# Kernel optimization log

Hardware: AMD Instinct MI355X
Metric: run time of the kernel (lower is better)

Reference implementation:

```python
import jax, jax.numpy as jnp
import numpy as np


def adder2d(x, w, stride=1, padding=0):
    """AdderNet conv: out = -sum_{ci,kh,kw} |x_patch - w|, supports groups.
    x: [B,Cin,H,W], w: [Cout, Cin//G, K, K]. Loops only over K*K kernel taps."""
    B, Cin, H, W = x.shape
    Cout, Cin_g, K, _ = w.shape
    G = Cin // Cin_g
    Co_g = Cout // G
    xp = jnp.pad(x, ((0, 0), (0, 0), (padding, padding), (padding, padding)))
    Ho = (H + 2 * padding - K) // stride + 1
    Wo = (W + 2 * padding - K) // stride + 1
    wg = w.reshape(G, Co_g, Cin_g, K, K)
    out = jnp.zeros((B, Cout, Ho, Wo), x.dtype)
    for kh in range(K):
        for kw in range(K):
            xs = jax.lax.slice(
                xp, (0, 0, kh, kw),
                (B, Cin, kh + stride * (Ho - 1) + 1, kw + stride * (Wo - 1) + 1),
                (1, 1, stride, stride))  # [B,Cin,Ho,Wo]
            xs = xs.reshape(B, G, 1, Cin_g, Ho, Wo)
            wt = wg[:, :, :, kh, kw][None, :, :, :, None, None]  # [1,G,Co_g,Cin_g,1,1]
            out = out - jnp.abs(xs - wt).sum(3).reshape(B, Cout, Ho, Wo)
    return out


def bn(x, g, b, m, v, eps=1e-5):
    inv = g / jnp.sqrt(v + eps)
    return x * inv[None, :, None, None] + (b - m * inv)[None, :, None, None]


def setup_inputs() -> dict:
    key = jax.random.key(0)
    ks = jax.random.split(key, 18)
    d = {}
    d["x"] = jax.random.normal(ks[0], (8, 256, 28, 28), jnp.float32)
    d["w1"] = jax.random.normal(ks[1], (64, 256, 1, 1), jnp.float32) * 0.05
    d["w_peg"] = jax.random.normal(ks[2], (64, 1, 3, 3), jnp.float32) * 0.05
    d["w2"] = jax.random.normal(ks[3], (64, 64, 3, 3), jnp.float32) * 0.05
    d["w3"] = jax.random.normal(ks[4], (256, 64, 1, 1), jnp.float32) * 0.05
    for i, (c, tag) in enumerate([(64, "1"), (64, "2"), (256, "3")]):
        d["g" + tag] = jax.random.uniform(ks[5 + 4 * i], (c,), jnp.float32, 0.5, 1.5)
        d["b" + tag] = jax.random.normal(ks[6 + 4 * i], (c,), jnp.float32) * 0.1
        d["m" + tag] = jax.random.normal(ks[7 + 4 * i], (c,), jnp.float32) * 0.1
        d["v" + tag] = jax.random.uniform(ks[8 + 4 * i], (c,), jnp.float32, 0.5, 1.5)
    return d


def reference(x, w1, w_peg, w2, w3, g1, b1, m1, v1, g2, b2, m2, v2, g3, b3, m3, v3):
    residual = x  # downsample is Identity (stride=1, inplanes==outplanes)
    h = adder2d(x, w1)                       # 1x1 adder conv 256->64
    h = adder2d(h, w_peg, stride=1, padding=1)  # PEG: depthwise 3x3 adder conv
    h = jax.nn.relu(bn(h, g1, b1, m1, v1))
    h = adder2d(h, w2, padding=1)            # 3x3 adder conv 64->64
    h = jax.nn.relu(bn(h, g2, b2, m2, v2))
    h = adder2d(h, w3)                       # 1x1 adder conv 64->256
    h = bn(h, g3, b3, m3, v3)
    return jax.nn.relu(h + residual)
```

## Files before the change

### kernel.cpp

```cpp
#include <hip/hip_runtime.h>
#include <math.h>

#define HW 28
#define PR 30
#define PC 32
#define PPAD (PR * PC)

#define OFF_H1P 0
#define OFF_H2P 491520
#define OFF_H3  983040
#define OFF_W2T 1384448
#define OFF_W3T 1421312
#define OFF_W1T 1437696

__device__ __forceinline__ void tap3(const float4 a, const float2 b,
                                     const float w0, const float w1, const float w2,
                                     float4& acc) {
    acc.x += fabsf(a.x - w0) + fabsf(a.y - w1) + fabsf(a.z - w2);
    acc.y += fabsf(a.y - w0) + fabsf(a.z - w1) + fabsf(a.w - w2);
    acc.z += fabsf(a.z - w0) + fabsf(a.w - w1) + fabsf(b.x - w2);
    acc.w += fabsf(a.w - w0) + fabsf(b.x - w1) + fabsf(b.y - w2);
}

__global__ __launch_bounds__(256) void k0_setup(const float* __restrict__ w1,
                                                const float* __restrict__ w2,
                                                const float* __restrict__ w3,
                                                float* __restrict__ w1t,
                                                float* __restrict__ w2t,
                                                float* __restrict__ w3t,
                                                float* __restrict__ h1p,
                                                float* __restrict__ h2p) {
    int t = blockIdx.x * 256 + threadIdx.x;
    if (t < 16384) {
        int ci = t >> 6, co = t & 63;
        w1t[t] = w1[co * 256 + ci];
    } else if (t < 53248) {
        int r2 = t - 16384;
        int r = r2 >> 6, co = r2 & 63;
        w2t[r2] = w2[(size_t)co * 576 + r];
    } else if (t < 69632) {
        int r3 = t - 53248;
        int ci = r3 >> 8, co = r3 & 255;
        w3t[r3] = w3[co * 64 + ci];
    } else {
        int h = t - 69632;
        float* buf = (h < 90112) ? h1p : h2p;
        int rem = (h < 90112) ? h : h - 90112;
        int plane = rem / 176, r = rem % 176;
        int row, col;
        if (r < 64) { row = (r >> 5) * 29; col = r & 31; }
        else { int j = r - 64; row = 1 + (j >> 2); int k = j & 3; col = k ? 28 + k : 0; }
        buf[(size_t)plane * PPAD + row * PC + col] = 0.f;
    }
}

__global__ __launch_bounds__(448) void k1_adder1x1(const float* __restrict__ x,
                                                   const float* __restrict__ w1t,
                                                   float* __restrict__ h1p) {
    __shared__ __align__(16) float smem[7168];
    float*  ws  = smem;
    float4* pl4 = (float4*)smem;
    const int tid    = threadIdx.x;
    const int cog    = tid & 3;
    const int pxg    = (tid >> 2) % 7;
    const int cic    = tid / 28;
    const int n      = blockIdx.x / 28;
    const int y      = blockIdx.x % 28;
    const int px0    = y * 28 + pxg * 4;
    const int cobase = blockIdx.y * 16;

    for (int idx = tid; idx < 4096; idx += 448) {
        int ci = idx >> 4, co = idx & 15;
        ws[ci * 20 + co] = w1t[ci * 64 + cobase + co];
    }
    __syncthreads();

    float4 acc0 = {0,0,0,0}, acc1 = acc0, acc2 = acc0, acc3 = acc0;
    const float* xp = x + ((size_t)n * 256 + cic * 16) * 784 + px0;
    const float* wp = ws + (cic * 16) * 20 + cog * 4;
    #pragma unroll 8
    for (int i = 0; i < 16; ++i) {
        float4 u = *(const float4*)(xp + (size_t)i * 784);
        float4 w = *(const float4*)(wp + i * 20);
        acc0.x += fabsf(u.x - w.x); acc0.y += fabsf(u.y - w.x); acc0.z += fabsf(u.z - w.x); acc0.w += fabsf(u.w - w.x);
        acc1.x += fabsf(u.x - w.y); acc1.y += fabsf(u.y - w.y); acc1.z += fabsf(u.z - w.y); acc1.w += fabsf(u.w - w.y);
        acc2.x += fabsf(u.x - w.z); acc2.y += fabsf(u.y - w.z); acc2.z += fabsf(u.z - w.z); acc2.w += fabsf(u.w - w.z);
        acc3.x += fabsf(u.x - w.w); acc3.y += fabsf(u.y - w.w); acc3.z += fabsf(u.z - w.w); acc3.w += fabsf(u.w - w.w);
    }
    __syncthreads();
    const int pbase = pxg * 16 + cog * 4;
    pl4[cic * 112 + pbase + 0] = acc0;
    pl4[cic * 112 + pbase + 1] = acc1;
    pl4[cic * 112 + pbase + 2] = acc2;
    pl4[cic * 112 + pbase + 3] = acc3;
    __syncthreads();

    if (tid < 112) {
        const int rpxg = tid >> 4;
        const int rcog = (tid >> 2) & 3;
        const int j    = tid & 3;
        const int rb   = rpxg * 16 + rcog * 4 + j;
        float4 s = pl4[rb];
        #pragma unroll
        for (int c = 1; c < 16; ++c) {
            float4 t = pl4[c * 112 + rb];
            s.x += t.x; s.y += t.y; s.z += t.z; s.w += t.w;
        }
        const int co = cobase + rcog * 4 + j;
        float* op = h1p + ((size_t)(n * 64 + co) * PR + y + 1) * PC + rpxg * 4 + 1;
        op[0] = -s.x; op[1] = -s.y; op[2] = -s.z; op[3] = -s.w;
    }
}

__global__ __launch_bounds__(256) void k2_peg_bn_relu(const float* __restrict__ h1p,
                                                      const float* __restrict__ wp,
                                                      const float* __restrict__ g1,
                                                      const float* __restrict__ b1,
                                                      const float* __restrict__ m1,
                                                      const float* __restrict__ v1,
                                                      float* __restrict__ h2p) {
    const int t   = blockIdx.x * 256 + threadIdx.x;
    const int pxq = t % 196;
    const int c   = (t / 196) & 63;
    const int n   = t / (196 * 64);
    const int p0  = pxq * 4;
    const int y   = p0 / 28, xx = p0 % 28;

    const float* base = h1p + ((size_t)(n * 64 + c) * PR + y) * PC + xx;
    const float* wc   = wp + c * 9;
    float4 acc = {0,0,0,0};
    #pragma unroll
    for (int kh = 0; kh < 3; ++kh) {
        float4 a = *(const float4*)(base + kh * PC);
        float2 b = *(const float2*)(base + kh * PC + 4);
        tap3(a, b, wc[kh * 3 + 0], wc[kh * 3 + 1], wc[kh * 3 + 2], acc);
    }
    float inv = g1[c] * rsqrtf(v1[c] + 1e-5f);
    float bb  = b1[c] - m1[c] * inv;
    float* op = h2p + ((size_t)(n * 64 + c) * PR + y + 1) * PC + xx + 1;
    op[0] = fmaxf(-acc.x * inv + bb, 0.f);
    op[1] = fmaxf(-acc.y * inv + bb, 0.f);
    op[2] = fmaxf(-acc.z * inv + bb, 0.f);
    op[3] = fmaxf(-acc.w * inv + bb, 0.f);
}

__global__ __launch_bounds__(448) void k3_adder3x3_bn_relu(const float* __restrict__ h2p,
                                                           const float* __restrict__ w2t,
                                                           const float* __restrict__ g2,
                                                           const float* __restrict__ b2,
                                                           const float* __restrict__ m2,
                                                           const float* __restrict__ v2,
                                                           float* __restrict__ h3) {
    __shared__ __align__(16) float smem[9216];
    float*  ws  = smem;
    float4* pl4 = (float4*)smem;
    const int tid    = threadIdx.x;
    const int cog    = tid & 3;
    const int pxg    = (tid >> 2) % 7;
    const int cic    = tid / 28;
    const int Y      = blockIdx.x;
    const int cobase = blockIdx.y * 16;
    const int n      = blockIdx.z;
    const int xx0    = pxg * 4;

    #pragma unroll
    for (int k = 0; k < 21; ++k) {
        int idx = tid + k * 448;
        if (idx < 9216) ws[idx] = w2t[(size_t)(idx >> 4) * 64 + cobase + (idx & 15)];
    }
    __syncthreads();

    float4 acc0 = {0,0,0,0}, acc1 = acc0, acc2 = acc0, acc3 = acc0;
    #pragma unroll 2
    for (int i = 0; i < 4; ++i) {
        const int ci = cic * 4 + i;
        const float* rp = h2p + (((size_t)(n * 64 + ci)) * PR + Y) * PC + xx0;
        const float* wr = ws + ci * 144 + cog * 4;
        #pragma unroll
        for (int kh = 0; kh < 3; ++kh) {
            float4 a = *(const float4*)(rp + kh * PC);
            float2 b = *(const float2*)(rp + kh * PC + 4);
            const float* wk = wr + kh * 48;
            float4 W0 = *(const float4*)(wk);
            float4 W1 = *(const float4*)(wk + 16);
            float4 W2 = *(const float4*)(wk + 32);
            tap3(a, b, W0.x, W1.x, W2.x, acc0);
            tap3(a, b, W0.y, W1.y, W2.y, acc1);
            tap3(a, b, W0.z, W1.z, W2.z, acc2);
            tap3(a, b, W0.w, W1.w, W2.w, acc3);
        }
    }
    __syncthreads();
    const int pbase = pxg * 16 + cog * 4;
    pl4[cic * 112 + pbase + 0] = acc0;
    pl4[cic * 112 + pbase + 1] = acc1;
    pl4[cic * 112 + pbase + 2] = acc2;
    pl4[cic * 112 + pbase + 3] = acc3;
    __syncthreads();

    if (tid < 112) {
        const int rpxg = tid >> 4;
        const int rcog = (tid >> 2) & 3;
        const int j    = tid & 3;
        const int rb   = rpxg * 16 + rcog * 4 + j;
        float4 s = pl4[rb];
        #pragma unroll
        for (int c = 1; c < 16; ++c) {
            float4 t = pl4[c * 112 + rb];
            s.x += t.x; s.y += t.y; s.z += t.z; s.w += t.w;
        }
        const int co = cobase + rcog * 4 + j;
        float inv = g2[co] * rsqrtf(v2[co] + 1e-5f);
        float bb  = b2[co] - m2[co] * inv;
        float4 o;
        o.x = fmaxf(-s.x * inv + bb, 0.f);
        o.y = fmaxf(-s.y * inv + bb, 0.f);
        o.z = fmaxf(-s.z * inv + bb, 0.f);
        o.w = fmaxf(-s.w * inv + bb, 0.f);
        *(float4*)(h3 + (size_t)(n * 64 + co) * 784 + Y * 28 + rpxg * 4) = o;
    }
}

__global__ __launch_bounds__(448) void k6_adder1x1_bn_res_relu(const float* __restrict__ h3,
                                                               const float* __restrict__ w3t,
                                                               const float* __restrict__ x,
                                                               const float* __restrict__ g3,
                                                               const float* __restrict__ b3,
                                                               const float* __restrict__ m3,
                                                               const float* __restrict__ v3,
                                                               float* __restrict__ out) {
    __shared__ __align__(16) float smem[7168];
    float*  ws  = smem;
    float4* pl4 = (float4*)smem;
    const int tid    = threadIdx.x;
    const int cog    = tid & 7;
    const int pxg    = (tid >> 3) % 14;
    const int cic    = tid / 112;
    const int n      = blockIdx.x / 14;
    const int p0     = (blockIdx.x % 14) * 56 + pxg * 4;
    const int cobase = blockIdx.y * 32;

    for (int idx = tid; idx < 2048; idx += 448) {
        int ci = idx >> 5, co = idx & 31;
        ws[ci * 36 + co] = w3t[ci * 256 + cobase + co];
    }
    __syncthreads();

    float4 acc0 = {0,0,0,0}, acc1 = acc0, acc2 = acc0, acc3 = acc0;
    const float* hp = h3 + ((size_t)n * 64 + cic * 16) * 784 + p0;
    const float* wp = ws + (cic * 16) * 36 + cog * 4;
    #pragma unroll 8
    for (int i = 0; i < 16; ++i) {
        float4 u = *(const float4*)(hp + (size_t)i * 784);
        float4 w = *(const float4*)(wp + i * 36);
        acc0.x += fabsf(u.x - w.x); acc0.y += fabsf(u.y - w.x); acc0.z += fabsf(u.z - w.x); acc0.w += fabsf(u.w - w.x);
        acc1.x += fabsf(u.x - w.y); acc1.y += fabsf(u.y - w.y); acc1.z += fabsf(u.z - w.y); acc1.w += fabsf(u.w - w.y);
        acc2.x += fabsf(u.x - w.z); acc2.y += fabsf(u.y - w.z); acc2.z += fabsf(u.z - w.z); acc2.w += fabsf(u.w - w.z);
        acc3.x += fabsf(u.x - w.w); acc3.y += fabsf(u.y - w.w); acc3.z += fabsf(u.z - w.w); acc3.w += fabsf(u.w - w.w);
    }
    __syncthreads();
    const int pbase = pxg * 32 + cog * 4;
    pl4[cic * 448 + pbase + 0] = acc0;
    pl4[cic * 448 + pbase + 1] = acc1;
    pl4[cic * 448 + pbase + 2] = acc2;
    pl4[cic * 448 + pbase + 3] = acc3;
    __syncthreads();

    {
        const int j = cic;
        float4 s = pl4[pbase + j];
        #pragma unroll
        for (int c = 1; c < 4; ++c) {
            float4 t = pl4[c * 448 + pbase + j];
            s.x += t.x; s.y += t.y; s.z += t.z; s.w += t.w;
        }
        const int co = cobase + cog * 4 + j;
        float inv = g3[co] * rsqrtf(v3[co] + 1e-5f);
        float bb  = b3[co] - m3[co] * inv;
        size_t obase = ((size_t)n * 256 + co) * 784 + p0;
        float4 r = *(const float4*)(x + obase);
        float4 o;
        o.x = fmaxf(-s.x * inv + bb + r.x, 0.f);
        o.y = fmaxf(-s.y * inv + bb + r.y, 0.f);
        o.z = fmaxf(-s.z * inv + bb + r.z, 0.f);
        o.w = fmaxf(-s.w * inv + bb + r.w, 0.f);
        *(float4*)(out + obase) = o;
    }
}

extern "C" void kernel_launch(void* const* d_in, const int* in_sizes, int n_in,
                              void* d_out, int out_size, void* d_ws, size_t ws_size,
                              hipStream_t stream) {
    const float* x  = (const float*)d_in[0];
    const float* w1 = (const float*)d_in[1];
    const float* wp = (const float*)d_in[2];
    const float* w2 = (const float*)d_in[3];
    const float* w3 = (const float*)d_in[4];
    const float* g1 = (const float*)d_in[5];
    const float* b1 = (const float*)d_in[6];
    const float* m1 = (const float*)d_in[7];
    const float* v1 = (const float*)d_in[8];
    const float* g2 = (const float*)d_in[9];
    const float* b2 = (const float*)d_in[10];
    const float* m2 = (const float*)d_in[11];
    const float* v2 = (const float*)d_in[12];
    const float* g3 = (const float*)d_in[13];
    const float* b3 = (const float*)d_in[14];
    const float* m3 = (const float*)d_in[15];
    const float* v3 = (const float*)d_in[16];
    float* out = (float*)d_out;

    float* wsf = (float*)d_ws;
    float* h1p = wsf + OFF_H1P;
    float* h2p = wsf + OFF_H2P;
    float* h3  = wsf + OFF_H3;
    float* w2t = wsf + OFF_W2T;
    float* w3t = wsf + OFF_W3T;
    float* w1t = wsf + OFF_W1T;

    k0_setup<<<dim3(976), 256, 0, stream>>>(w1, w2, w3, w1t, w2t, w3t, h1p, h2p);
    k1_adder1x1<<<dim3(224, 4), 448, 0, stream>>>(x, w1t, h1p);
    k2_peg_bn_relu<<<dim3(392), 256, 0, stream>>>(h1p, wp, g1, b1, m1, v1, h2p);
    k3_adder3x3_bn_relu<<<dim3(28, 4, 8), 448, 0, stream>>>(h2p, w2t, g2, b2, m2, v2, h3);
    k6_adder1x1_bn_res_relu<<<dim3(112, 8), 448, 0, stream>>>(h3, w3t, x, g3, b3, m3, v3, out);
}
```

Baseline: 69.81 us.

## Drop setup kernel; fold weight transposes and halo zeroing into consumers, retile 3x3

```diff
diff --git a/kernel.cpp b/kernel.cpp
--- a/kernel.cpp
+++ b/kernel.cpp
@@ -9,9 +9,6 @@
 #define OFF_H1P 0
 #define OFF_H2P 491520
 #define OFF_H3  983040
-#define OFF_W2T 1384448
-#define OFF_W3T 1421312
-#define OFF_W1T 1437696
 
 __device__ __forceinline__ void tap3(const float4 a, const float2 b,
                                      const float w0, const float w1, const float w2,
@@ -22,40 +19,8 @@
     acc.w += fabsf(a.w - w0) + fabsf(b.x - w1) + fabsf(b.y - w2);
 }
 
-__global__ __launch_bounds__(256) void k0_setup(const float* __restrict__ w1,
-                                                const float* __restrict__ w2,
-                                                const float* __restrict__ w3,
-                                                float* __restrict__ w1t,
-                                                float* __restrict__ w2t,
-                                                float* __restrict__ w3t,
-                                                float* __restrict__ h1p,
-                                                float* __restrict__ h2p) {
-    int t = blockIdx.x * 256 + threadIdx.x;
-    if (t < 16384) {
-        int ci = t >> 6, co = t & 63;
-        w1t[t] = w1[co * 256 + ci];
-    } else if (t < 53248) {
-        int r2 = t - 16384;
-        int r = r2 >> 6, co = r2 & 63;
-        w2t[r2] = w2[(size_t)co * 576 + r];
-    } else if (t < 69632) {
-        int r3 = t - 53248;
-        int ci = r3 >> 8, co = r3 & 255;
-        w3t[r3] = w3[co * 64 + ci];
-    } else {
-        int h = t - 69632;
-        float* buf = (h < 90112) ? h1p : h2p;
-        int rem = (h < 90112) ? h : h - 90112;
-        int plane = rem / 176, r = rem % 176;
-        int row, col;
-        if (r < 64) { row = (r >> 5) * 29; col = r & 31; }
-        else { int j = r - 64; row = 1 + (j >> 2); int k = j & 3; col = k ? 28 + k : 0; }
-        buf[(size_t)plane * PPAD + row * PC + col] = 0.f;
-    }
-}
-
 __global__ __launch_bounds__(448) void k1_adder1x1(const float* __restrict__ x,
-                                                   const float* __restrict__ w1t,
+                                                   const float* __restrict__ w1,
                                                    float* __restrict__ h1p) {
     __shared__ __align__(16) float smem[7168];
     float*  ws  = smem;
@@ -70,8 +35,8 @@
     const int cobase = blockIdx.y * 16;
 
     for (int idx = tid; idx < 4096; idx += 448) {
-        int ci = idx >> 4, co = idx & 15;
-        ws[ci * 20 + co] = w1t[ci * 64 + cobase + co];
+        int co = idx >> 8, ci = idx & 255;
+        ws[ci * 20 + co] = w1[(size_t)(cobase + co) * 256 + ci];
     }
     __syncthreads();
 
@@ -109,6 +74,15 @@
         const int co = cobase + rcog * 4 + j;
         float* op = h1p + ((size_t)(n * 64 + co) * PR + y + 1) * PC + rpxg * 4 + 1;
         op[0] = -s.x; op[1] = -s.y; op[2] = -s.z; op[3] = -s.w;
+        if (rpxg == 0) op[-1] = 0.f;
+        if (rpxg == 6) { op[4] = 0.f; op[5] = 0.f; op[6] = 0.f; }
+    }
+    if (y == 0 || y == 27) {
+        const int prow = (y == 0) ? 0 : 29;
+        for (int idx = tid; idx < 512; idx += 448) {
+            int coi = idx >> 5, col = idx & 31;
+            h1p[((size_t)(n * 64 + cobase + coi) * PR + prow) * PC + col] = 0.f;
+        }
     }
 }
 
@@ -119,71 +93,81 @@
                                                       const float* __restrict__ m1,
                                                       const float* __restrict__ v1,
                                                       float* __restrict__ h2p) {
-    const int t   = blockIdx.x * 256 + threadIdx.x;
-    const int pxq = t % 196;
-    const int c   = (t / 196) & 63;
-    const int n   = t / (196 * 64);
-    const int p0  = pxq * 4;
-    const int y   = p0 / 28, xx = p0 % 28;
-
-    const float* base = h1p + ((size_t)(n * 64 + c) * PR + y) * PC + xx;
-    const float* wc   = wp + c * 9;
-    float4 acc = {0,0,0,0};
-    #pragma unroll
-    for (int kh = 0; kh < 3; ++kh) {
-        float4 a = *(const float4*)(base + kh * PC);
-        float2 b = *(const float2*)(base + kh * PC + 4);
-        tap3(a, b, wc[kh * 3 + 0], wc[kh * 3 + 1], wc[kh * 3 + 2], acc);
-    }
-    float inv = g1[c] * rsqrtf(v1[c] + 1e-5f);
-    float bb  = b1[c] - m1[c] * inv;
-    float* op = h2p + ((size_t)(n * 64 + c) * PR + y + 1) * PC + xx + 1;
-    op[0] = fmaxf(-acc.x * inv + bb, 0.f);
-    op[1] = fmaxf(-acc.y * inv + bb, 0.f);
-    op[2] = fmaxf(-acc.z * inv + bb, 0.f);
-    op[3] = fmaxf(-acc.w * inv + bb, 0.f);
+    const int t = blockIdx.x * 256 + threadIdx.x;
+    if (t < 100352) {
+        const int pxq = t % 196;
+        const int c   = (t / 196) & 63;
+        const int n   = t / (196 * 64);
+        const int p0  = pxq * 4;
+        const int y   = p0 / 28, xx = p0 % 28;
+        const float* base = h1p + ((size_t)(n * 64 + c) * PR + y) * PC + xx;
+        const float* wc   = wp + c * 9;
+        float4 acc = {0,0,0,0};
+        #pragma unroll
+        for (int kh = 0; kh < 3; ++kh) {
+            float4 a = *(const float4*)(base + kh * PC);
+            float2 b = *(const float2*)(base + kh * PC + 4);
+            tap3(a, b, wc[kh * 3 + 0], wc[kh * 3 + 1], wc[kh * 3 + 2], acc);
+        }
+        float inv = g1[c] * rsqrtf(v1[c] + 1e-5f);
+        float bb  = b1[c] - m1[c] * inv;
+        float* op = h2p + ((size_t)(n * 64 + c) * PR + y + 1) * PC + xx + 1;
+        op[0] = fmaxf(-acc.x * inv + bb, 0.f);
+        op[1] = fmaxf(-acc.y * inv + bb, 0.f);
+        op[2] = fmaxf(-acc.z * inv + bb, 0.f);
+        op[3] = fmaxf(-acc.w * inv + bb, 0.f);
+    } else {
+        int i = t - 100352;
+        int plane = i / 176, r = i % 176;
+        int row, col;
+        if (r < 64) { row = (r >> 5) * 29; col = r & 31; }
+        else { int j = r - 64; row = 1 + (j >> 2); int k = j & 3; col = k ? 28 + k : 0; }
+        h2p[(size_t)plane * PPAD + row * PC + col] = 0.f;
+    }
 }
 
 __global__ __launch_bounds__(448) void k3_adder3x3_bn_relu(const float* __restrict__ h2p,
-                                                           const float* __restrict__ w2t,
+                                                           const float* __restrict__ w2,
                                                            const float* __restrict__ g2,
                                                            const float* __restrict__ b2,
                                                            const float* __restrict__ m2,
                                                            const float* __restrict__ v2,
                                                            float* __restrict__ h3) {
-    __shared__ __align__(16) float smem[9216];
+    __shared__ __align__(16) float smem[11520];
     float*  ws  = smem;
     float4* pl4 = (float4*)smem;
     const int tid    = threadIdx.x;
     const int cog    = tid & 3;
-    const int pxg    = (tid >> 2) % 7;
-    const int cic    = tid / 28;
-    const int Y      = blockIdx.x;
+    const int pxg    = (tid >> 2) % 14;
+    const int cic    = tid / 56;
+    const int y0     = blockIdx.x * 2;
     const int cobase = blockIdx.y * 16;
     const int n      = blockIdx.z;
-    const int xx0    = pxg * 4;
-
-    #pragma unroll
-    for (int k = 0; k < 21; ++k) {
-        int idx = tid + k * 448;
-        if (idx < 9216) ws[idx] = w2t[(size_t)(idx >> 4) * 64 + cobase + (idx & 15)];
+    const int yl     = pxg / 7;
+    const int xx0    = (pxg % 7) * 4;
+    const int Y      = y0 + yl;
+
+    for (int idx = tid; idx < 9216; idx += 448) {
+        int co = idx / 576;
+        int r  = idx - co * 576;
+        ws[r * 20 + co] = w2[(size_t)(cobase + co) * 576 + r];
     }
     __syncthreads();
 
     float4 acc0 = {0,0,0,0}, acc1 = acc0, acc2 = acc0, acc3 = acc0;
     #pragma unroll 2
-    for (int i = 0; i < 4; ++i) {
-        const int ci = cic * 4 + i;
+    for (int i = 0; i < 8; ++i) {
+        const int ci = cic * 8 + i;
         const float* rp = h2p + (((size_t)(n * 64 + ci)) * PR + Y) * PC + xx0;
-        const float* wr = ws + ci * 144 + cog * 4;
+        const float* wr = ws + ci * 180 + cog * 4;
         #pragma unroll
         for (int kh = 0; kh < 3; ++kh) {
             float4 a = *(const float4*)(rp + kh * PC);
             float2 b = *(const float2*)(rp + kh * PC + 4);
-            const float* wk = wr + kh * 48;
+            const float* wk = wr + kh * 60;
             float4 W0 = *(const float4*)(wk);
-            float4 W1 = *(const float4*)(wk + 16);
-            float4 W2 = *(const float4*)(wk + 32);
+            float4 W1 = *(const float4*)(wk + 20);
+            float4 W2 = *(const float4*)(wk + 40);
             tap3(a, b, W0.x, W1.x, W2.x, acc0);
             tap3(a, b, W0.y, W1.y, W2.y, acc1);
             tap3(a, b, W0.z, W1.z, W2.z, acc2);
@@ -192,24 +176,21 @@
     }
     __syncthreads();
     const int pbase = pxg * 16 + cog * 4;
-    pl4[cic * 112 + pbase + 0] = acc0;
-    pl4[cic * 112 + pbase + 1] = acc1;
-    pl4[cic * 112 + pbase + 2] = acc2;
-    pl4[cic * 112 + pbase + 3] = acc3;
-    __syncthreads();
-
-    if (tid < 112) {
-        const int rpxg = tid >> 4;
-        const int rcog = (tid >> 2) & 3;
-        const int j    = tid & 3;
-        const int rb   = rpxg * 16 + rcog * 4 + j;
-        float4 s = pl4[rb];
-        #pragma unroll
-        for (int c = 1; c < 16; ++c) {
-            float4 t = pl4[c * 112 + rb];
+    pl4[cic * 224 + pbase + 0] = acc0;
+    pl4[cic * 224 + pbase + 1] = acc1;
+    pl4[cic * 224 + pbase + 2] = acc2;
+    pl4[cic * 224 + pbase + 3] = acc3;
+    __syncthreads();
+
+    if (tid < 224) {
+        const int j = cic;
+        float4 s = pl4[pbase + j];
+        #pragma unroll
+        for (int c = 1; c < 8; ++c) {
+            float4 t = pl4[c * 224 + pbase + j];
             s.x += t.x; s.y += t.y; s.z += t.z; s.w += t.w;
         }
-        const int co = cobase + rcog * 4 + j;
+        const int co = cobase + cog * 4 + j;
         float inv = g2[co] * rsqrtf(v2[co] + 1e-5f);
         float bb  = b2[co] - m2[co] * inv;
         float4 o;
@@ -217,12 +198,12 @@
         o.y = fmaxf(-s.y * inv + bb, 0.f);
         o.z = fmaxf(-s.z * inv + bb, 0.f);
         o.w = fmaxf(-s.w * inv + bb, 0.f);
-        *(float4*)(h3 + (size_t)(n * 64 + co) * 784 + Y * 28 + rpxg * 4) = o;
+        *(float4*)(h3 + (size_t)(n * 64 + co) * 784 + Y * 28 + xx0) = o;
     }
 }
 
 __global__ __launch_bounds__(448) void k6_adder1x1_bn_res_relu(const float* __restrict__ h3,
-                                                               const float* __restrict__ w3t,
+                                                               const float* __restrict__ w3,
                                                                const float* __restrict__ x,
                                                                const float* __restrict__ g3,
                                                                const float* __restrict__ b3,
@@ -241,8 +222,8 @@
     const int cobase = blockIdx.y * 32;
 
     for (int idx = tid; idx < 2048; idx += 448) {
-        int ci = idx >> 5, co = idx & 31;
-        ws[ci * 36 + co] = w3t[ci * 256 + cobase + co];
+        int co = idx >> 6, ci = idx & 63;
+        ws[ci * 36 + co] = w3[(size_t)(cobase + co) * 64 + ci];
     }
     __syncthreads();
 
@@ -314,13 +295,9 @@
     float* h1p = wsf + OFF_H1P;
     float* h2p = wsf + OFF_H2P;
     float* h3  = wsf + OFF_H3;
-    float* w2t = wsf + OFF_W2T;
-    float* w3t = wsf + OFF_W3T;
-    float* w1t = wsf + OFF_W1T;
-
-    k0_setup<<<dim3(976), 256, 0, stream>>>(w1, w2, w3, w1t, w2t, w3t, h1p, h2p);
-    k1_adder1x1<<<dim3(224, 4), 448, 0, stream>>>(x, w1t, h1p);
-    k2_peg_bn_relu<<<dim3(392), 256, 0, stream>>>(h1p, wp, g1, b1, m1, v1, h2p);
-    k3_adder3x3_bn_relu<<<dim3(28, 4, 8), 448, 0, stream>>>(h2p, w2t, g2, b2, m2, v2, h3);
-    k6_adder1x1_bn_res_relu<<<dim3(112, 8), 448, 0, stream>>>(h3, w3t, x, g3, b3, m3, v3, out);
-}
+
+    k1_adder1x1<<<dim3(224, 4), 448, 0, stream>>>(x, w1, h1p);
+    k2_peg_bn_relu<<<dim3(744), 256, 0, stream>>>(h1p, wp, g1, b1, m1, v1, h2p);
+    k3_adder3x3_bn_relu<<<dim3(14, 4, 8), 448, 0, stream>>>(h2p, w2, g2, b2, m2, v2, h3);
+    k6_adder1x1_bn_res_relu<<<dim3(112, 8), 448, 0, stream>>>(h3, w3, x, g3, b3, m3, v3, out);
+}
```

New measurement: 66.81 us. -4.3%, faster.
